# Kernel tuning notes

Measured on AMD Instinct MI355X. Metric: run time of the kernel, lower is better.

The kernel has to match this reference:

```python
import jax, jax.numpy as jnp
import numpy as np

N_NODES = 100000
N_EDGES = 1600000
IN_F, HID_F, OUT_F = 128, 128, 64


def setup_inputs() -> dict:
    key = jax.random.key(0)
    ks = jax.random.split(key, 10)
    x = jax.random.normal(ks[0], (N_NODES, IN_F), dtype=jnp.float32)
    adj_row = jax.random.randint(ks[1], (N_EDGES,), 0, N_NODES, dtype=jnp.int64)
    adj_col = jax.random.randint(ks[2], (N_EDGES,), 0, N_NODES, dtype=jnp.int64)
    adj_val = jax.random.uniform(ks[3], (N_EDGES,), dtype=jnp.float32)
    # layer weights (xavier-normal-ish scale), stored as [in, out]
    def w(k, fin, fout):
        return jax.random.normal(k, (fin, fout), dtype=jnp.float32) * jnp.sqrt(2.0 / (fin + fout))
    return {
        "x": x, "adj_row": adj_row, "adj_col": adj_col, "adj_val": adj_val,
        "W0": w(ks[4], IN_F, HID_F), "b0": jnp.zeros((HID_F,), jnp.float32),
        "W1": w(ks[5], HID_F, HID_F), "b1": jnp.zeros((HID_F,), jnp.float32),
        "W2": w(ks[6], HID_F, OUT_F), "b2": jnp.zeros((OUT_F,), jnp.float32),
    }


def _spmm(adj_row, adj_col, adj_val, h):
    # sparse [N,N] @ dense [N,F]: gather source rows, scale, scatter-add to dest
    msgs = adj_val[:, None] * h[adj_col]            # [E, F]
    return jax.ops.segment_sum(msgs, adj_row, num_segments=N_NODES)


def reference(x, adj_row, adj_col, adj_val, W0, b0, W1, b1, W2, b2):
    h = x
    params = [(W0, b0), (W1, b1), (W2, b2)]
    n_layers = len(params)
    for i, (W, b) in enumerate(params):
        h = h @ W + b                               # Linear
        h = _spmm(adj_row, adj_col, adj_val, h)     # torch.sparse.mm(adj, h)
        if i != n_layers - 1:
            h = jax.nn.relu(h)                      # activation on hidden layers only
    return h


if __name__ == "__main__":
    out = reference(**setup_inputs())
    print(out.shape)
```

## Files before the change

kernel.cpp:

```cpp
#include <hip/hip_runtime.h>
#include <hip/hip_bf16.h>

#define N_NODES 100000
#define N_EDGES 1600000

#define BIN_SHIFT 9
#define NBIN 196
#define NBLK 256
#define CHUNK 6250
#define SCAN_N (NBIN * NBLK)

typedef __attribute__((ext_vector_type(8))) short bf16x8;
typedef __attribute__((ext_vector_type(4))) float f32x4;

__device__ inline unsigned short f2bf(float f) {
    union { float f; unsigned u; } v; v.f = f;
    unsigned r = v.u + 0x7FFF + ((v.u >> 16) & 1);
    return (unsigned short)(r >> 16);
}
__device__ inline float bf2f(unsigned short h) {
    union { unsigned u; float f; } v; v.u = ((unsigned)h) << 16;
    return v.f;
}


__global__ __launch_bounds__(256) void p1_bincnt(const int* __restrict__ row,
                                                 int* __restrict__ cnt) {
    __shared__ int h[NBIN];
    for (int i = threadIdx.x; i < NBIN; i += 256) h[i] = 0;
    __syncthreads();
    int base = blockIdx.x * CHUNK;
    int end = base + CHUNK; if (end > N_EDGES) end = N_EDGES;
    for (int i = base + threadIdx.x; i < end; i += 256)
        atomicAdd(&h[row[i] >> BIN_SHIFT], 1);
    __syncthreads();
    for (int b = threadIdx.x; b < NBIN; b += 256)
        cnt[b * NBLK + blockIdx.x] = h[b];
}

__global__ __launch_bounds__(1024) void p2_scan(const int* __restrict__ cnt,
                                                int* __restrict__ base,
                                                int* __restrict__ rp) {
    __shared__ int s[1024];
    int t = threadIdx.x;
    const int per = SCAN_N / 1024;
    int lo = t * per, hi = lo + per;
    int sum = 0;
    for (int i = lo; i < hi; ++i) sum += cnt[i];
    s[t] = sum;
    __syncthreads();
    for (int off = 1; off < 1024; off <<= 1) {
        int v = (t >= off) ? s[t - off] : 0;
        __syncthreads();
        s[t] += v;
        __syncthreads();
    }
    int run = s[t] - sum;
    for (int i = lo; i < hi; ++i) { int c = cnt[i]; base[i] = run; run += c; }
    if (t == 0) rp[N_NODES] = N_EDGES;
}

__global__ __launch_bounds__(256) void p3_partition(const int* __restrict__ row,
                                                    const int* __restrict__ col,
                                                    const float* __restrict__ val,
                                                    const int* __restrict__ base,
                                                    int2* __restrict__ bout) {
    __shared__ int cur[NBIN];
    for (int i = threadIdx.x; i < NBIN; i += 256)
        cur[i] = base[i * NBLK + blockIdx.x];
    __syncthreads();
    int lo = blockIdx.x * CHUNK;
    int end = lo + CHUNK; if (end > N_EDGES) end = N_EDGES;
    for (int i = lo + threadIdx.x; i < end; i += 256) {
        int r = row[i];
        int b = r >> BIN_SHIFT;
        int p = atomicAdd(&cur[b], 1);
        int2 rec;
        rec.x = col[i] | ((r & 511) << 17);
        rec.y = __float_as_int(val[i]);
        bout[p] = rec;
    }
}

__global__ __launch_bounds__(256) void p4_binscatter(const int* __restrict__ base,
                                                     const int2* __restrict__ bin_in,
                                                     int* __restrict__ rp,
                                                     int2* __restrict__ erec) {
    __shared__ int cnt[512];
    __shared__ int part[256];
    const int b = blockIdx.x;
    const int t = threadIdx.x;
    const int lo = base[b * NBLK];
    const int hi = (b + 1 < NBIN) ? base[(b + 1) * NBLK] : N_EDGES;

    cnt[t] = 0; cnt[t + 256] = 0;
    __syncthreads();
    for (int e = lo + t; e < hi; e += 256)
        atomicAdd(&cnt[(unsigned)bin_in[e].x >> 17], 1);
    __syncthreads();

    int s0 = cnt[2 * t], s1 = cnt[2 * t + 1];
    int tsum = s0 + s1;
    part[t] = tsum;
    __syncthreads();
    for (int off = 1; off < 256; off <<= 1) {
        int v = (t >= off) ? part[t - off] : 0;
        __syncthreads();
        part[t] += v;
        __syncthreads();
    }
    int run = part[t] - tsum;
    cnt[2 * t] = run;
    cnt[2 * t + 1] = run + s0;

    const int rowbase = b << BIN_SHIFT;
    int r0 = rowbase + 2 * t, r1 = rowbase + 2 * t + 1;
    if (r0 < N_NODES) rp[r0] = lo + run;
    if (r1 < N_NODES) rp[r1] = lo + run + s0;
    __syncthreads();

    for (int e = lo + t; e < hi; e += 256) {
        int2 q = bin_in[e];
        int rl = (unsigned)q.x >> 17;
        int p = lo + atomicAdd(&cnt[rl], 1);
        int2 rec;
        rec.x = q.x & 0x1FFFF;
        rec.y = q.y;
        erec[p] = rec;
    }
}


template<int FOUT>
__global__ void pack_w_kernel(const float* __restrict__ W, unsigned short* __restrict__ Bp) {
    int idx = blockIdx.x * blockDim.x + threadIdx.x;
    if (idx >= FOUT * 128) return;
    int j = idx & 7, lane = (idx >> 3) & 63, kb = (idx >> 9) & 3, nt = idx >> 11;
    int k = kb * 32 + (lane >> 4) * 8 + j;
    int col = nt * 16 + (lane & 15);
    Bp[idx] = f2bf(W[k * FOUT + col]);
}


template<int FOUT, bool AF32>
__global__ __launch_bounds__(256) void gemm_mfma(const void* __restrict__ Xv,
                                                 const unsigned short* __restrict__ Bp,
                                                 const float* __restrict__ bias,
                                                 unsigned short* __restrict__ Y, int n) {
    const int wave = threadIdx.x >> 6;
    const int lane = threadIdx.x & 63;
    const int l15 = lane & 15, kg = lane >> 4;
    const int nbase = blockIdx.y * 64;
    const int rowTile = blockIdx.x * 128 + wave * 32;

    int r0 = rowTile + l15;      if (r0 >= n) r0 = n - 1;
    int r1 = rowTile + 16 + l15; if (r1 >= n) r1 = n - 1;

    bf16x8 a0[4], a1[4];
    if constexpr (AF32) {
        const float* x0 = (const float*)Xv + (size_t)r0 * 128 + kg * 8;
        const float* x1 = (const float*)Xv + (size_t)r1 * 128 + kg * 8;
        #pragma unroll
        for (int kb = 0; kb < 4; ++kb) {
            float4 u = *reinterpret_cast<const float4*>(x0 + kb * 32);
            float4 v = *reinterpret_cast<const float4*>(x0 + kb * 32 + 4);
            a0[kb] = (bf16x8){(short)f2bf(u.x), (short)f2bf(u.y), (short)f2bf(u.z), (short)f2bf(u.w),
                              (short)f2bf(v.x), (short)f2bf(v.y), (short)f2bf(v.z), (short)f2bf(v.w)};
            float4 p = *reinterpret_cast<const float4*>(x1 + kb * 32);
            float4 q = *reinterpret_cast<const float4*>(x1 + kb * 32 + 4);
            a1[kb] = (bf16x8){(short)f2bf(p.x), (short)f2bf(p.y), (short)f2bf(p.z), (short)f2bf(p.w),
                              (short)f2bf(q.x), (short)f2bf(q.y), (short)f2bf(q.z), (short)f2bf(q.w)};
        }
    } else {
        const bf16x8* x0 = reinterpret_cast<const bf16x8*>((const unsigned short*)Xv + (size_t)r0 * 128 + kg * 8);
        const bf16x8* x1 = reinterpret_cast<const bf16x8*>((const unsigned short*)Xv + (size_t)r1 * 128 + kg * 8);
        #pragma unroll
        for (int kb = 0; kb < 4; ++kb) { a0[kb] = x0[kb * 4]; a1[kb] = x1[kb * 4]; }
    }

    f32x4 c0[4], c1[4];
    #pragma unroll
    for (int t = 0; t < 4; ++t) {
        c0[t] = (f32x4){0.f, 0.f, 0.f, 0.f};
        c1[t] = (f32x4){0.f, 0.f, 0.f, 0.f};
    }

    const bf16x8* bpv = reinterpret_cast<const bf16x8*>(Bp);
    #pragma unroll
    for (int nt = 0; nt < 4; ++nt) {
        int ntAbs = (nbase >> 4) + nt;
        const bf16x8* bp = bpv + (size_t)(ntAbs * 4) * 64 + lane;
        #pragma unroll
        for (int kb = 0; kb < 4; ++kb) {
            bf16x8 b = bp[kb * 64];
            c0[nt] = __builtin_amdgcn_mfma_f32_16x16x32_bf16(a0[kb], b, c0[nt], 0, 0, 0);
            c1[nt] = __builtin_amdgcn_mfma_f32_16x16x32_bf16(a1[kb], b, c1[nt], 0, 0, 0);
        }
    }

    #pragma unroll
    for (int nt = 0; nt < 4; ++nt) {
        int col = nbase + nt * 16 + l15;
        float bv = bias[col];
        int rb = rowTile + kg * 4;
        #pragma unroll
        for (int j = 0; j < 4; ++j) {
            int ra = rb + j;
            if (ra < n) Y[(size_t)ra * FOUT + col] = f2bf(c0[nt][j] + bv);
            int rc = rb + 16 + j;
            if (rc < n) Y[(size_t)rc * FOUT + col] = f2bf(c1[nt][j] + bv);
        }
    }
}


__global__ __launch_bounds__(256) void spmm_mid(const int* __restrict__ rp,
                                                const int2* __restrict__ erec,
                                                const unsigned int* __restrict__ G,
                                                unsigned int* __restrict__ Y, int n) {
    int node = blockIdx.x * 4 + (threadIdx.x >> 6);
    if (node >= n) return;
    int f = threadIdx.x & 63;
    int e0 = rp[node], e1 = rp[node + 1];
    float acc0 = 0.f, acc1 = 0.f;
    const unsigned* Gf = G + f;
    int e = e0;
    for (; e + 4 <= e1; e += 4) {
        int2 q0 = erec[e], q1 = erec[e + 1], q2 = erec[e + 2], q3 = erec[e + 3];
        unsigned g0 = Gf[(size_t)q0.x * 64];
        unsigned g1 = Gf[(size_t)q1.x * 64];
        unsigned g2 = Gf[(size_t)q2.x * 64];
        unsigned g3 = Gf[(size_t)q3.x * 64];
        float v0 = __int_as_float(q0.y), v1 = __int_as_float(q1.y);
        float v2 = __int_as_float(q2.y), v3 = __int_as_float(q3.y);
        acc0 += v0 * bf2f((unsigned short)g0) + v1 * bf2f((unsigned short)g1)
              + v2 * bf2f((unsigned short)g2) + v3 * bf2f((unsigned short)g3);
        acc1 += v0 * bf2f((unsigned short)(g0 >> 16)) + v1 * bf2f((unsigned short)(g1 >> 16))
              + v2 * bf2f((unsigned short)(g2 >> 16)) + v3 * bf2f((unsigned short)(g3 >> 16));
    }
    for (; e < e1; ++e) {
        int2 q = erec[e];
        float v = __int_as_float(q.y);
        unsigned g = Gf[(size_t)q.x * 64];
        acc0 += v * bf2f((unsigned short)g);
        acc1 += v * bf2f((unsigned short)(g >> 16));
    }
    acc0 = fmaxf(acc0, 0.f); acc1 = fmaxf(acc1, 0.f);
    Y[(size_t)node * 64 + f] = (unsigned)f2bf(acc0) | ((unsigned)f2bf(acc1) << 16);
}

__global__ __launch_bounds__(256) void spmm_last(const int* __restrict__ rp,
                                                 const int2* __restrict__ erec,
                                                 const unsigned short* __restrict__ G,
                                                 float* __restrict__ Y, int n) {
    int node = blockIdx.x * 4 + (threadIdx.x >> 6);
    if (node >= n) return;
    int f = threadIdx.x & 63;
    int e0 = rp[node], e1 = rp[node + 1];
    float acc = 0.f;
    const unsigned short* Gf = G + f;
    int e = e0;
    for (; e + 4 <= e1; e += 4) {
        int2 q0 = erec[e], q1 = erec[e + 1], q2 = erec[e + 2], q3 = erec[e + 3];
        acc += __int_as_float(q0.y) * bf2f(Gf[(size_t)q0.x * 64])
             + __int_as_float(q1.y) * bf2f(Gf[(size_t)q1.x * 64])
             + __int_as_float(q2.y) * bf2f(Gf[(size_t)q2.x * 64])
             + __int_as_float(q3.y) * bf2f(Gf[(size_t)q3.x * 64]);
    }
    for (; e < e1; ++e) {
        int2 q = erec[e];
        acc += __int_as_float(q.y) * bf2f(Gf[(size_t)q.x * 64]);
    }
    Y[(size_t)node * 64 + f] = acc;
}


extern "C" void kernel_launch(void* const* d_in, const int* in_sizes, int n_in,
                              void* d_out, int out_size, void* d_ws, size_t ws_size,
                              hipStream_t stream) {
    const float* x    = (const float*)d_in[0];
    const int*   arow = (const int*)d_in[1];
    const int*   acol = (const int*)d_in[2];
    const float* aval = (const float*)d_in[3];
    const float* W0   = (const float*)d_in[4];
    const float* b0   = (const float*)d_in[5];
    const float* W1   = (const float*)d_in[6];
    const float* b1   = (const float*)d_in[7];
    const float* W2   = (const float*)d_in[8];
    const float* b2   = (const float*)d_in[9];
    float* out = (float*)d_out;

    unsigned short* hlin = (unsigned short*)d_ws;
    unsigned short* hact = hlin + (size_t)N_NODES * 128;
    unsigned short* Bp0  = hact + (size_t)N_NODES * 128;
    unsigned short* Bp1  = Bp0 + 128 * 128;
    unsigned short* Bp2  = Bp1 + 128 * 128;
    int* cnt   = (int*)(Bp2 + 64 * 128);
    int* base  = cnt + SCAN_N;
    int* rp    = base + SCAN_N;
    int2* bin_in = (int2*)(rp + N_NODES + 2);
    int2* erec   = bin_in + N_EDGES;

    p1_bincnt<<<NBLK, 256, 0, stream>>>(arow, cnt);
    p2_scan<<<1, 1024, 0, stream>>>(cnt, base, rp);
    p3_partition<<<NBLK, 256, 0, stream>>>(arow, acol, aval, base, bin_in);
    p4_binscatter<<<NBIN, 256, 0, stream>>>(base, bin_in, rp, erec);

    pack_w_kernel<128><<<64, 256, 0, stream>>>(W0, Bp0);
    pack_w_kernel<128><<<64, 256, 0, stream>>>(W1, Bp1);
    pack_w_kernel<64><<<32, 256, 0, stream>>>(W2, Bp2);

    dim3 gemm_grid((N_NODES + 127) / 128, 2);
    dim3 gemm_grid2((N_NODES + 127) / 128, 1);
    int spmm_grid = (N_NODES + 3) / 4;

    gemm_mfma<128, true><<<gemm_grid, 256, 0, stream>>>(x, Bp0, b0, hlin, N_NODES);
    spmm_mid<<<spmm_grid, 256, 0, stream>>>(rp, erec, (const unsigned*)hlin, (unsigned*)hact, N_NODES);
    gemm_mfma<128, false><<<gemm_grid, 256, 0, stream>>>(hact, Bp1, b1, hlin, N_NODES);
    spmm_mid<<<spmm_grid, 256, 0, stream>>>(rp, erec, (const unsigned*)hlin, (unsigned*)hact, N_NODES);
    gemm_mfma<64, false><<<gemm_grid2, 256, 0, stream>>>(hact, Bp2, b2, hlin, N_NODES);
    spmm_last<<<spmm_grid, 256, 0, stream>>>(rp, erec, hlin, out, N_NODES);
}
```

Before: 350.7 us.

## Fuse SpMM aggregation with following layer's MFMA GEMM through shared memory

Replaces the mid-layer spmm kernels and the following GEMMs with a fused kernel that aggregates 128 nodes' neighbor rows into an LDS tile (with ReLU and bf16 packing), then runs MFMA against the next weight matrix and writes the bf16 result directly. This removes one global write and read of the intermediate activation per layer and two kernel launches. The gather now uses wider 8-byte loads with edges split across two half-waves, combined by a lane shuffle, and spmm_last is restructured the same way. The trade-off is fewer blocks (one per 128 nodes) with serialized per-row gathers per wave and heavier LDS use per block, which may reduce latency hiding on the irregular gather.

```diff
diff --git a/kernel.cpp b/kernel.cpp
--- a/kernel.cpp
+++ b/kernel.cpp
@@ -130,7 +130,6 @@
     }
 }
 
-
 template<int FOUT>
 __global__ void pack_w_kernel(const float* __restrict__ W, unsigned short* __restrict__ Bp) {
     int idx = blockIdx.x * blockDim.x + threadIdx.x;
@@ -142,11 +141,11 @@
 }
 
 
-template<int FOUT, bool AF32>
-__global__ __launch_bounds__(256) void gemm_mfma(const void* __restrict__ Xv,
-                                                 const unsigned short* __restrict__ Bp,
-                                                 const float* __restrict__ bias,
-                                                 unsigned short* __restrict__ Y, int n) {
+template<int FOUT>
+__global__ __launch_bounds__(256) void gemm_mfma_f32A(const float* __restrict__ X,
+                                                      const unsigned short* __restrict__ Bp,
+                                                      const float* __restrict__ bias,
+                                                      unsigned short* __restrict__ Y, int n) {
     const int wave = threadIdx.x >> 6;
     const int lane = threadIdx.x & 63;
     const int l15 = lane & 15, kg = lane >> 4;
@@ -157,25 +156,18 @@
     int r1 = rowTile + 16 + l15; if (r1 >= n) r1 = n - 1;
 
     bf16x8 a0[4], a1[4];
-    if constexpr (AF32) {
-        const float* x0 = (const float*)Xv + (size_t)r0 * 128 + kg * 8;
-        const float* x1 = (const float*)Xv + (size_t)r1 * 128 + kg * 8;
-        #pragma unroll
-        for (int kb = 0; kb < 4; ++kb) {
-            float4 u = *reinterpret_cast<const float4*>(x0 + kb * 32);
-            float4 v = *reinterpret_cast<const float4*>(x0 + kb * 32 + 4);
-            a0[kb] = (bf16x8){(short)f2bf(u.x), (short)f2bf(u.y), (short)f2bf(u.z), (short)f2bf(u.w),
-                              (short)f2bf(v.x), (short)f2bf(v.y), (short)f2bf(v.z), (short)f2bf(v.w)};
-            float4 p = *reinterpret_cast<const float4*>(x1 + kb * 32);
-            float4 q = *reinterpret_cast<const float4*>(x1 + kb * 32 + 4);
-            a1[kb] = (bf16x8){(short)f2bf(p.x), (short)f2bf(p.y), (short)f2bf(p.z), (short)f2bf(p.w),
-                              (short)f2bf(q.x), (short)f2bf(q.y), (short)f2bf(q.z), (short)f2bf(q.w)};
-        }
-    } else {
-        const bf16x8* x0 = reinterpret_cast<const bf16x8*>((const unsigned short*)Xv + (size_t)r0 * 128 + kg * 8);
-        const bf16x8* x1 = reinterpret_cast<const bf16x8*>((const unsigned short*)Xv + (size_t)r1 * 128 + kg * 8);
-        #pragma unroll
-        for (int kb = 0; kb < 4; ++kb) { a0[kb] = x0[kb * 4]; a1[kb] = x1[kb * 4]; }
+    const float* x0 = X + (size_t)r0 * 128 + kg * 8;
+    const float* x1 = X + (size_t)r1 * 128 + kg * 8;
+    #pragma unroll
+    for (int kb = 0; kb < 4; ++kb) {
+        float4 u = *reinterpret_cast<const float4*>(x0 + kb * 32);
+        float4 v = *reinterpret_cast<const float4*>(x0 + kb * 32 + 4);
+        a0[kb] = (bf16x8){(short)f2bf(u.x), (short)f2bf(u.y), (short)f2bf(u.z), (short)f2bf(u.w),
+                          (short)f2bf(v.x), (short)f2bf(v.y), (short)f2bf(v.z), (short)f2bf(v.w)};
+        float4 p = *reinterpret_cast<const float4*>(x1 + kb * 32);
+        float4 q = *reinterpret_cast<const float4*>(x1 + kb * 32 + 4);
+        a1[kb] = (bf16x8){(short)f2bf(p.x), (short)f2bf(p.y), (short)f2bf(p.z), (short)f2bf(p.w),
+                          (short)f2bf(q.x), (short)f2bf(q.y), (short)f2bf(q.z), (short)f2bf(q.w)};
     }
 
     f32x4 c0[4], c1[4];
@@ -214,64 +206,132 @@
 }
 
 
-__global__ __launch_bounds__(256) void spmm_mid(const int* __restrict__ rp,
-                                                const int2* __restrict__ erec,
-                                                const unsigned int* __restrict__ G,
-                                                unsigned int* __restrict__ Y, int n) {
-    int node = blockIdx.x * 4 + (threadIdx.x >> 6);
-    if (node >= n) return;
-    int f = threadIdx.x & 63;
-    int e0 = rp[node], e1 = rp[node + 1];
-    float acc0 = 0.f, acc1 = 0.f;
-    const unsigned* Gf = G + f;
-    int e = e0;
-    for (; e + 4 <= e1; e += 4) {
-        int2 q0 = erec[e], q1 = erec[e + 1], q2 = erec[e + 2], q3 = erec[e + 3];
-        unsigned g0 = Gf[(size_t)q0.x * 64];
-        unsigned g1 = Gf[(size_t)q1.x * 64];
-        unsigned g2 = Gf[(size_t)q2.x * 64];
-        unsigned g3 = Gf[(size_t)q3.x * 64];
-        float v0 = __int_as_float(q0.y), v1 = __int_as_float(q1.y);
-        float v2 = __int_as_float(q2.y), v3 = __int_as_float(q3.y);
-        acc0 += v0 * bf2f((unsigned short)g0) + v1 * bf2f((unsigned short)g1)
-              + v2 * bf2f((unsigned short)g2) + v3 * bf2f((unsigned short)g3);
-        acc1 += v0 * bf2f((unsigned short)(g0 >> 16)) + v1 * bf2f((unsigned short)(g1 >> 16))
-              + v2 * bf2f((unsigned short)(g2 >> 16)) + v3 * bf2f((unsigned short)(g3 >> 16));
-    }
-    for (; e < e1; ++e) {
-        int2 q = erec[e];
-        float v = __int_as_float(q.y);
-        unsigned g = Gf[(size_t)q.x * 64];
-        acc0 += v * bf2f((unsigned short)g);
-        acc1 += v * bf2f((unsigned short)(g >> 16));
-    }
-    acc0 = fmaxf(acc0, 0.f); acc1 = fmaxf(acc1, 0.f);
-    Y[(size_t)node * 64 + f] = (unsigned)f2bf(acc0) | ((unsigned)f2bf(acc1) << 16);
-}
+template<int FOUT>
+__global__ __launch_bounds__(512, 4) void spmm_gemm_fused(const int* __restrict__ rp,
+                                                          const int2* __restrict__ erec,
+                                                          const unsigned* __restrict__ G,
+                                                          const unsigned short* __restrict__ Bp,
+                                                          const float* __restrict__ bias,
+                                                          unsigned short* __restrict__ Y,
+                                                          int n) {
+    __shared__ unsigned short A[128 * 136];
+    const int wave = threadIdx.x >> 6;
+    const int lane = threadIdx.x & 63;
+    const int half = lane >> 5;
+    const int f2 = lane & 31;
+    const int tile = blockIdx.x * 128;
+
+    for (int i = 0; i < 16; ++i) {
+        int lrow = wave * 16 + i;
+        int node = tile + lrow;
+        float a0 = 0.f, a1 = 0.f, a2 = 0.f, a3 = 0.f;
+        if (node < n) {
+            int e0 = rp[node], e1 = rp[node + 1];
+            int e = e0 + half;
+            for (; e + 3 <= e1; e += 4) {
+                int2 qa = erec[e], qb = erec[e + 2];
+                uint2 ga = *reinterpret_cast<const uint2*>(G + (size_t)qa.x * 64 + f2 * 2);
+                uint2 gb = *reinterpret_cast<const uint2*>(G + (size_t)qb.x * 64 + f2 * 2);
+                float va = __int_as_float(qa.y), vb = __int_as_float(qb.y);
+                a0 += va * bf2f((unsigned short)ga.x) + vb * bf2f((unsigned short)gb.x);
+                a1 += va * bf2f((unsigned short)(ga.x >> 16)) + vb * bf2f((unsigned short)(gb.x >> 16));
+                a2 += va * bf2f((unsigned short)ga.y) + vb * bf2f((unsigned short)gb.y);
+                a3 += va * bf2f((unsigned short)(ga.y >> 16)) + vb * bf2f((unsigned short)(gb.y >> 16));
+            }
+            if (e < e1) {
+                int2 q = erec[e];
+                uint2 g = *reinterpret_cast<const uint2*>(G + (size_t)q.x * 64 + f2 * 2);
+                float v = __int_as_float(q.y);
+                a0 += v * bf2f((unsigned short)g.x);
+                a1 += v * bf2f((unsigned short)(g.x >> 16));
+                a2 += v * bf2f((unsigned short)g.y);
+                a3 += v * bf2f((unsigned short)(g.y >> 16));
+            }
+        }
+        a0 += __shfl_xor(a0, 32);
+        a1 += __shfl_xor(a1, 32);
+        a2 += __shfl_xor(a2, 32);
+        a3 += __shfl_xor(a3, 32);
+        if (half == 0) {
+            a0 = fmaxf(a0, 0.f); a1 = fmaxf(a1, 0.f);
+            a2 = fmaxf(a2, 0.f); a3 = fmaxf(a3, 0.f);
+            unsigned p0 = (unsigned)f2bf(a0) | ((unsigned)f2bf(a1) << 16);
+            unsigned p1 = (unsigned)f2bf(a2) | ((unsigned)f2bf(a3) << 16);
+            uint2 pk; pk.x = p0; pk.y = p1;
+            *reinterpret_cast<uint2*>(&A[lrow * 136 + f2 * 4]) = pk;
+        }
+    }
+    __syncthreads();
+
+    const int l15 = lane & 15, kg = lane >> 4;
+    bf16x8 afr[4];
+    const unsigned short* arow = &A[(wave * 16 + l15) * 136 + kg * 8];
+    #pragma unroll
+    for (int kb = 0; kb < 4; ++kb)
+        afr[kb] = *reinterpret_cast<const bf16x8*>(arow + kb * 32);
+
+    constexpr int NT = FOUT / 16;
+    f32x4 c[NT];
+    #pragma unroll
+    for (int nt = 0; nt < NT; ++nt) c[nt] = (f32x4){0.f, 0.f, 0.f, 0.f};
+
+    const bf16x8* bpv = reinterpret_cast<const bf16x8*>(Bp);
+    #pragma unroll
+    for (int nt = 0; nt < NT; ++nt) {
+        const bf16x8* bp = bpv + (size_t)(nt * 4) * 64 + lane;
+        #pragma unroll
+        for (int kb = 0; kb < 4; ++kb)
+            c[nt] = __builtin_amdgcn_mfma_f32_16x16x32_bf16(afr[kb], bp[kb * 64], c[nt], 0, 0, 0);
+    }
+
+    #pragma unroll
+    for (int nt = 0; nt < NT; ++nt) {
+        int col = nt * 16 + l15;
+        float bv = bias[col];
+        int rb = tile + wave * 16 + kg * 4;
+        #pragma unroll
+        for (int j = 0; j < 4; ++j) {
+            int r = rb + j;
+            if (r < n) Y[(size_t)r * FOUT + col] = f2bf(c[nt][j] + bv);
+        }
+    }
+}
+
 
 __global__ __launch_bounds__(256) void spmm_last(const int* __restrict__ rp,
                                                  const int2* __restrict__ erec,
-                                                 const unsigned short* __restrict__ G,
+                                                 const unsigned* __restrict__ G,
                                                  float* __restrict__ Y, int n) {
     int node = blockIdx.x * 4 + (threadIdx.x >> 6);
     if (node >= n) return;
-    int f = threadIdx.x & 63;
+    int lane = threadIdx.x & 63;
+    int half = lane >> 5;
+    int f2 = lane & 31;
     int e0 = rp[node], e1 = rp[node + 1];
-    float acc = 0.f;
-    const unsigned short* Gf = G + f;
-    int e = e0;
-    for (; e + 4 <= e1; e += 4) {
-        int2 q0 = erec[e], q1 = erec[e + 1], q2 = erec[e + 2], q3 = erec[e + 3];
-        acc += __int_as_float(q0.y) * bf2f(Gf[(size_t)q0.x * 64])
-             + __int_as_float(q1.y) * bf2f(Gf[(size_t)q1.x * 64])
-             + __int_as_float(q2.y) * bf2f(Gf[(size_t)q2.x * 64])
-             + __int_as_float(q3.y) * bf2f(Gf[(size_t)q3.x * 64]);
-    }
-    for (; e < e1; ++e) {
+    float a0 = 0.f, a1 = 0.f;
+    const unsigned* Gf = G + f2;
+    int e = e0 + half;
+    for (; e + 3 <= e1; e += 4) {
+        int2 qa = erec[e], qb = erec[e + 2];
+        unsigned ga = Gf[(size_t)qa.x * 32];
+        unsigned gb = Gf[(size_t)qb.x * 32];
+        float va = __int_as_float(qa.y), vb = __int_as_float(qb.y);
+        a0 += va * bf2f((unsigned short)ga) + vb * bf2f((unsigned short)gb);
+        a1 += va * bf2f((unsigned short)(ga >> 16)) + vb * bf2f((unsigned short)(gb >> 16));
+    }
+    if (e < e1) {
         int2 q = erec[e];
-        acc += __int_as_float(q.y) * bf2f(Gf[(size_t)q.x * 64]);
-    }
-    Y[(size_t)node * 64 + f] = acc;
+        unsigned g = Gf[(size_t)q.x * 32];
+        float v = __int_as_float(q.y);
+        a0 += v * bf2f((unsigned short)g);
+        a1 += v * bf2f((unsigned short)(g >> 16));
+    }
+    a0 += __shfl_xor(a0, 32);
+    a1 += __shfl_xor(a1, 32);
+    if (half == 0) {
+        float2 o; o.x = a0; o.y = a1;
+        *reinterpret_cast<float2*>(&Y[(size_t)node * 64 + f2 * 2]) = o;
+    }
 }
 
 
@@ -290,9 +350,9 @@
     const float* b2   = (const float*)d_in[9];
     float* out = (float*)d_out;
 
-    unsigned short* hlin = (unsigned short*)d_ws;
-    unsigned short* hact = hlin + (size_t)N_NODES * 128;
-    unsigned short* Bp0  = hact + (size_t)N_NODES * 128;
+    unsigned short* hbuf0 = (unsigned short*)d_ws;
+    unsigned short* hbuf1 = hbuf0 + (size_t)N_NODES * 128;
+    unsigned short* Bp0  = hbuf1 + (size_t)N_NODES * 128;
     unsigned short* Bp1  = Bp0 + 128 * 128;
     unsigned short* Bp2  = Bp1 + 128 * 128;
     int* cnt   = (int*)(Bp2 + 64 * 128);
@@ -311,13 +371,11 @@
     pack_w_kernel<64><<<32, 256, 0, stream>>>(W2, Bp2);
 
     dim3 gemm_grid((N_NODES + 127) / 128, 2);
-    dim3 gemm_grid2((N_NODES + 127) / 128, 1);
+    int fused_grid = (N_NODES + 127) / 128;
     int spmm_grid = (N_NODES + 3) / 4;
 
-    gemm_mfma<128, true><<<gemm_grid, 256, 0, stream>>>(x, Bp0, b0, hlin, N_NODES);
-    spmm_mid<<<spmm_grid, 256, 0, stream>>>(rp, erec, (const unsigned*)hlin, (unsigned*)hact, N_NODES);
-    gemm_mfma<128, false><<<gemm_grid, 256, 0, stream>>>(hact, Bp1, b1, hlin, N_NODES);
-    spmm_mid<<<spmm_grid, 256, 0, stream>>>(rp, erec, (const unsigned*)hlin, (unsigned*)hact, N_NODES);
-    gemm_mfma<64, false><<<gemm_grid2, 256, 0, stream>>>(hact, Bp2, b2, hlin, N_NODES);
-    spmm_last<<<spmm_grid, 256, 0, stream>>>(rp, erec, hlin, out, N_NODES);
-}
+    gemm_mfma_f32A<128><<<gemm_grid, 256, 0, stream>>>(x, Bp0, b0, hbuf0, N_NODES);
+    spmm_gemm_fused<128><<<fused_grid, 512, 0, stream>>>(rp, erec, (const unsigned*)hbuf0, Bp1, b1, hbuf1, N_NODES);
+    spmm_gemm_fused<64><<<fused_grid, 512, 0, stream>>>(rp, erec, (const unsigned*)hbuf1, Bp2, b2, hbuf0, N_NODES);
+    spmm_last<<<spmm_grid, 256, 0, stream>>>(rp, erec, (const unsigned*)hbuf0, out, N_NODES);
+}
```

New measurement: 392.7 us. +12.0%, slower.

## Slice feature matrices into 16-column panels and compress edge records to 32 bits

Applied to the files above, without the earlier changes.

Intermediate activations are now stored in a sliced layout of 16-feature panels, each N×16 bf16, so the gather for a given panel reads a compact 32-byte row per source node and stays cache-resident. SpMM kernels process one panel per block, with 8 lanes per edge group and cross-lane shuffles to reduce partial sums. Edge records are packed into 32 bits (17-bit column plus 15-bit truncated bf16 value), which halves edge traffic but lowers the precision of the adjacency values. The three weight-packing launches are merged into one.

```diff
diff --git a/kernel.cpp b/kernel.cpp
--- a/kernel.cpp
+++ b/kernel.cpp
@@ -3,6 +3,8 @@
 
 #define N_NODES 100000
 #define N_EDGES 1600000
+#define N16 (N_NODES * 16)
+#define N8  (N_NODES * 8)
 
 #define BIN_SHIFT 9
 #define NBIN 196
@@ -20,6 +22,10 @@
 }
 __device__ inline float bf2f(unsigned short h) {
     union { unsigned u; float f; } v; v.u = ((unsigned)h) << 16;
+    return v.f;
+}
+__device__ inline float recval(unsigned q) {
+    union { unsigned u; float f; } v; v.u = (q & 0x7FFFu) << 17;
     return v.f;
 }
 
@@ -85,7 +91,7 @@
 __global__ __launch_bounds__(256) void p4_binscatter(const int* __restrict__ base,
                                                      const int2* __restrict__ bin_in,
                                                      int* __restrict__ rp,
-                                                     int2* __restrict__ erec) {
+                                                     unsigned* __restrict__ erec) {
     __shared__ int cnt[512];
     __shared__ int part[256];
     const int b = blockIdx.x;
@@ -123,26 +129,32 @@
         int2 q = bin_in[e];
         int rl = (unsigned)q.x >> 17;
         int p = lo + atomicAdd(&cnt[rl], 1);
-        int2 rec;
-        rec.x = q.x & 0x1FFFF;
-        rec.y = q.y;
+        unsigned rec = ((unsigned)(q.x & 0x1FFFF) << 15)
+                     | (((unsigned)f2bf(__int_as_float(q.y))) >> 1);
         erec[p] = rec;
     }
 }
 
 
-template<int FOUT>
-__global__ void pack_w_kernel(const float* __restrict__ W, unsigned short* __restrict__ Bp) {
-    int idx = blockIdx.x * blockDim.x + threadIdx.x;
-    if (idx >= FOUT * 128) return;
-    int j = idx & 7, lane = (idx >> 3) & 63, kb = (idx >> 9) & 3, nt = idx >> 11;
+__global__ __launch_bounds__(256) void pack_all(const float* __restrict__ W0,
+                                                const float* __restrict__ W1,
+                                                const float* __restrict__ W2,
+                                                unsigned short* __restrict__ Bp0,
+                                                unsigned short* __restrict__ Bp1,
+                                                unsigned short* __restrict__ Bp2) {
+    int idx = blockIdx.x * 256 + threadIdx.x;
+    const float* W; unsigned short* Bp; int fout, li;
+    if (idx < 16384)      { W = W0; Bp = Bp0; fout = 128; li = idx; }
+    else if (idx < 32768) { W = W1; Bp = Bp1; fout = 128; li = idx - 16384; }
+    else                  { W = W2; Bp = Bp2; fout = 64;  li = idx - 32768; }
+    int j = li & 7, lane = (li >> 3) & 63, kb = (li >> 9) & 3, nt = li >> 11;
     int k = kb * 32 + (lane >> 4) * 8 + j;
     int col = nt * 16 + (lane & 15);
-    Bp[idx] = f2bf(W[k * FOUT + col]);
-}
-
-
-template<int FOUT, bool AF32>
+    Bp[li] = f2bf(W[k * fout + col]);
+}
+
+
+template<int FOUT, int AMODE>
 __global__ __launch_bounds__(256) void gemm_mfma(const void* __restrict__ Xv,
                                                  const unsigned short* __restrict__ Bp,
                                                  const float* __restrict__ bias,
@@ -157,7 +169,7 @@
     int r1 = rowTile + 16 + l15; if (r1 >= n) r1 = n - 1;
 
     bf16x8 a0[4], a1[4];
-    if constexpr (AF32) {
+    if constexpr (AMODE == 0) {
         const float* x0 = (const float*)Xv + (size_t)r0 * 128 + kg * 8;
         const float* x1 = (const float*)Xv + (size_t)r1 * 128 + kg * 8;
         #pragma unroll
@@ -172,10 +184,13 @@
                               (short)f2bf(q.x), (short)f2bf(q.y), (short)f2bf(q.z), (short)f2bf(q.w)};
         }
     } else {
-        const bf16x8* x0 = reinterpret_cast<const bf16x8*>((const unsigned short*)Xv + (size_t)r0 * 128 + kg * 8);
-        const bf16x8* x1 = reinterpret_cast<const bf16x8*>((const unsigned short*)Xv + (size_t)r1 * 128 + kg * 8);
+        const unsigned short* Xs = (const unsigned short*)Xv;
         #pragma unroll
-        for (int kb = 0; kb < 4; ++kb) { a0[kb] = x0[kb * 4]; a1[kb] = x1[kb * 4]; }
+        for (int kb = 0; kb < 4; ++kb) {
+            const unsigned short* bse = Xs + (size_t)(kb * 2 + (kg >> 1)) * N16 + (kg & 1) * 8;
+            a0[kb] = *reinterpret_cast<const bf16x8*>(bse + (size_t)r0 * 16);
+            a1[kb] = *reinterpret_cast<const bf16x8*>(bse + (size_t)r1 * 16);
+        }
     }
 
     f32x4 c0[4], c1[4];
@@ -202,76 +217,110 @@
     for (int nt = 0; nt < 4; ++nt) {
         int col = nbase + nt * 16 + l15;
         float bv = bias[col];
+        unsigned short* yb = Y + (size_t)((nbase >> 4) + nt) * N16 + l15;
         int rb = rowTile + kg * 4;
         #pragma unroll
         for (int j = 0; j < 4; ++j) {
             int ra = rb + j;
-            if (ra < n) Y[(size_t)ra * FOUT + col] = f2bf(c0[nt][j] + bv);
+            if (ra < n) yb[(size_t)ra * 16] = f2bf(c0[nt][j] + bv);
             int rc = rb + 16 + j;
-            if (rc < n) Y[(size_t)rc * FOUT + col] = f2bf(c1[nt][j] + bv);
-        }
-    }
-}
-
-
-__global__ __launch_bounds__(256) void spmm_mid(const int* __restrict__ rp,
-                                                const int2* __restrict__ erec,
-                                                const unsigned int* __restrict__ G,
-                                                unsigned int* __restrict__ Y, int n) {
-    int node = blockIdx.x * 4 + (threadIdx.x >> 6);
-    if (node >= n) return;
-    int f = threadIdx.x & 63;
-    int e0 = rp[node], e1 = rp[node + 1];
-    float acc0 = 0.f, acc1 = 0.f;
-    const unsigned* Gf = G + f;
-    int e = e0;
-    for (; e + 4 <= e1; e += 4) {
-        int2 q0 = erec[e], q1 = erec[e + 1], q2 = erec[e + 2], q3 = erec[e + 3];
-        unsigned g0 = Gf[(size_t)q0.x * 64];
-        unsigned g1 = Gf[(size_t)q1.x * 64];
-        unsigned g2 = Gf[(size_t)q2.x * 64];
-        unsigned g3 = Gf[(size_t)q3.x * 64];
-        float v0 = __int_as_float(q0.y), v1 = __int_as_float(q1.y);
-        float v2 = __int_as_float(q2.y), v3 = __int_as_float(q3.y);
-        acc0 += v0 * bf2f((unsigned short)g0) + v1 * bf2f((unsigned short)g1)
-              + v2 * bf2f((unsigned short)g2) + v3 * bf2f((unsigned short)g3);
-        acc1 += v0 * bf2f((unsigned short)(g0 >> 16)) + v1 * bf2f((unsigned short)(g1 >> 16))
-              + v2 * bf2f((unsigned short)(g2 >> 16)) + v3 * bf2f((unsigned short)(g3 >> 16));
-    }
-    for (; e < e1; ++e) {
-        int2 q = erec[e];
-        float v = __int_as_float(q.y);
-        unsigned g = Gf[(size_t)q.x * 64];
-        acc0 += v * bf2f((unsigned short)g);
-        acc1 += v * bf2f((unsigned short)(g >> 16));
-    }
-    acc0 = fmaxf(acc0, 0.f); acc1 = fmaxf(acc1, 0.f);
-    Y[(size_t)node * 64 + f] = (unsigned)f2bf(acc0) | ((unsigned)f2bf(acc1) << 16);
-}
-
-__global__ __launch_bounds__(256) void spmm_last(const int* __restrict__ rp,
-                                                 const int2* __restrict__ erec,
-                                                 const unsigned short* __restrict__ G,
-                                                 float* __restrict__ Y, int n) {
-    int node = blockIdx.x * 4 + (threadIdx.x >> 6);
-    if (node >= n) return;
-    int f = threadIdx.x & 63;
-    int e0 = rp[node], e1 = rp[node + 1];
-    float acc = 0.f;
-    const unsigned short* Gf = G + f;
-    int e = e0;
-    for (; e + 4 <= e1; e += 4) {
-        int2 q0 = erec[e], q1 = erec[e + 1], q2 = erec[e + 2], q3 = erec[e + 3];
-        acc += __int_as_float(q0.y) * bf2f(Gf[(size_t)q0.x * 64])
-             + __int_as_float(q1.y) * bf2f(Gf[(size_t)q1.x * 64])
-             + __int_as_float(q2.y) * bf2f(Gf[(size_t)q2.x * 64])
-             + __int_as_float(q3.y) * bf2f(Gf[(size_t)q3.x * 64]);
-    }
-    for (; e < e1; ++e) {
-        int2 q = erec[e];
-        acc += __int_as_float(q.y) * bf2f(Gf[(size_t)q.x * 64]);
-    }
-    Y[(size_t)node * 64 + f] = acc;
+            if (rc < n) yb[(size_t)rc * 16] = f2bf(c1[nt][j] + bv);
+        }
+    }
+}
+
+
+__global__ __launch_bounds__(256) void spmm_mid_sliced(const int* __restrict__ rp,
+                                                       const unsigned* __restrict__ erec,
+                                                       const unsigned* __restrict__ G,
+                                                       unsigned* __restrict__ Y,
+                                                       int n) {
+    const int slice = blockIdx.x & 7;
+    const int grp = blockIdx.x >> 3;
+    const int wave = threadIdx.x >> 6;
+    const int lane = threadIdx.x & 63;
+    const int sub = lane & 7;
+    const int eg = lane >> 3;
+    const unsigned* Gs = G + (size_t)slice * N8 + sub;
+    unsigned* Ys = Y + (size_t)slice * N8 + sub;
+    const int node0 = grp * 32 + wave * 8;
+
+    for (int i = 0; i < 8; ++i) {
+        int node = node0 + i;
+        if (node >= n) return;
+        int e0 = rp[node], e1 = rp[node + 1];
+        float f0 = 0.f, f1 = 0.f;
+        int e = e0 + eg;
+        for (; e + 8 < e1; e += 16) {
+            unsigned qa = __builtin_nontemporal_load(erec + e);
+            unsigned qb = __builtin_nontemporal_load(erec + e + 8);
+            unsigned ga = Gs[(size_t)(qa >> 15) * 8];
+            unsigned gb = Gs[(size_t)(qb >> 15) * 8];
+            float va = recval(qa), vb = recval(qb);
+            f0 += va * bf2f((unsigned short)ga) + vb * bf2f((unsigned short)gb);
+            f1 += va * bf2f((unsigned short)(ga >> 16)) + vb * bf2f((unsigned short)(gb >> 16));
+        }
+        if (e < e1) {
+            unsigned q = __builtin_nontemporal_load(erec + e);
+            unsigned g = Gs[(size_t)(q >> 15) * 8];
+            float v = recval(q);
+            f0 += v * bf2f((unsigned short)g);
+            f1 += v * bf2f((unsigned short)(g >> 16));
+        }
+        f0 += __shfl_xor(f0, 8);  f0 += __shfl_xor(f0, 16);  f0 += __shfl_xor(f0, 32);
+        f1 += __shfl_xor(f1, 8);  f1 += __shfl_xor(f1, 16);  f1 += __shfl_xor(f1, 32);
+        if (eg == 0) {
+            f0 = fmaxf(f0, 0.f); f1 = fmaxf(f1, 0.f);
+            unsigned pk = (unsigned)f2bf(f0) | ((unsigned)f2bf(f1) << 16);
+            __builtin_nontemporal_store(pk, Ys + (size_t)node * 8);
+        }
+    }
+}
+
+
+__global__ __launch_bounds__(256) void spmm_last_sliced(const int* __restrict__ rp,
+                                                        const unsigned* __restrict__ erec,
+                                                        const unsigned* __restrict__ G,
+                                                        float* __restrict__ out,
+                                                        int n) {
+    const int slice = blockIdx.x & 3;
+    const int grp = blockIdx.x >> 2;
+    const int wave = threadIdx.x >> 6;
+    const int lane = threadIdx.x & 63;
+    const int sub = lane & 7;
+    const int eg = lane >> 3;
+    const unsigned* Gs = G + (size_t)slice * N8 + sub;
+    const int node0 = grp * 32 + wave * 8;
+
+    for (int i = 0; i < 8; ++i) {
+        int node = node0 + i;
+        if (node >= n) return;
+        int e0 = rp[node], e1 = rp[node + 1];
+        float f0 = 0.f, f1 = 0.f;
+        int e = e0 + eg;
+        for (; e + 8 < e1; e += 16) {
+            unsigned qa = __builtin_nontemporal_load(erec + e);
+            unsigned qb = __builtin_nontemporal_load(erec + e + 8);
+            unsigned ga = Gs[(size_t)(qa >> 15) * 8];
+            unsigned gb = Gs[(size_t)(qb >> 15) * 8];
+            float va = recval(qa), vb = recval(qb);
+            f0 += va * bf2f((unsigned short)ga) + vb * bf2f((unsigned short)gb);
+            f1 += va * bf2f((unsigned short)(ga >> 16)) + vb * bf2f((unsigned short)(gb >> 16));
+        }
+        if (e < e1) {
+            unsigned q = __builtin_nontemporal_load(erec + e);
+            unsigned g = Gs[(size_t)(q >> 15) * 8];
+            float v = recval(q);
+            f0 += v * bf2f((unsigned short)g);
+            f1 += v * bf2f((unsigned short)(g >> 16));
+        }
+        f0 += __shfl_xor(f0, 8);  f0 += __shfl_xor(f0, 16);  f0 += __shfl_xor(f0, 32);
+        f1 += __shfl_xor(f1, 8);  f1 += __shfl_xor(f1, 16);  f1 += __shfl_xor(f1, 32);
+        if (eg == 0) {
+            float2 o; o.x = f0; o.y = f1;
+            *reinterpret_cast<float2*>(&out[(size_t)node * 64 + slice * 16 + sub * 2]) = o;
+        }
+    }
 }
 
 
@@ -290,34 +339,34 @@
     const float* b2   = (const float*)d_in[9];
     float* out = (float*)d_out;
 
-    unsigned short* hlin = (unsigned short*)d_ws;
-    unsigned short* hact = hlin + (size_t)N_NODES * 128;
-    unsigned short* Bp0  = hact + (size_t)N_NODES * 128;
-    unsigned short* Bp1  = Bp0 + 128 * 128;
-    unsigned short* Bp2  = Bp1 + 128 * 128;
-    int* cnt   = (int*)(Bp2 + 64 * 128);
-    int* base  = cnt + SCAN_N;
-    int* rp    = base + SCAN_N;
-    int2* bin_in = (int2*)(rp + N_NODES + 2);
-    int2* erec   = bin_in + N_EDGES;
+    unsigned short* S0  = (unsigned short*)d_ws;
+    unsigned short* S1  = S0 + (size_t)N_NODES * 128;
+    unsigned short* S2  = S1 + (size_t)N_NODES * 128;
+    unsigned short* Bp0 = S2 + (size_t)N_NODES * 64;
+    unsigned short* Bp1 = Bp0 + 16384;
+    unsigned short* Bp2 = Bp1 + 16384;
+    int* cnt  = (int*)(Bp2 + 8192);
+    int* base = cnt + SCAN_N;
+    int* rp   = base + SCAN_N;
+    int2* bin_in  = (int2*)(rp + N_NODES + 2);
+    unsigned* erec = (unsigned*)(bin_in + N_EDGES);
 
     p1_bincnt<<<NBLK, 256, 0, stream>>>(arow, cnt);
     p2_scan<<<1, 1024, 0, stream>>>(cnt, base, rp);
     p3_partition<<<NBLK, 256, 0, stream>>>(arow, acol, aval, base, bin_in);
     p4_binscatter<<<NBIN, 256, 0, stream>>>(base, bin_in, rp, erec);
 
-    pack_w_kernel<128><<<64, 256, 0, stream>>>(W0, Bp0);
-    pack_w_kernel<128><<<64, 256, 0, stream>>>(W1, Bp1);
-    pack_w_kernel<64><<<32, 256, 0, stream>>>(W2, Bp2);
+    pack_all<<<160, 256, 0, stream>>>(W0, W1, W2, Bp0, Bp1, Bp2);
 
     dim3 gemm_grid((N_NODES + 127) / 128, 2);
     dim3 gemm_grid2((N_NODES + 127) / 128, 1);
-    int spmm_grid = (N_NODES + 3) / 4;
-
-    gemm_mfma<128, true><<<gemm_grid, 256, 0, stream>>>(x, Bp0, b0, hlin, N_NODES);
-    spmm_mid<<<spmm_grid, 256, 0, stream>>>(rp, erec, (const unsigned*)hlin, (unsigned*)hact, N_NODES);
-    gemm_mfma<128, false><<<gemm_grid, 256, 0, stream>>>(hact, Bp1, b1, hlin, N_NODES);
-    spmm_mid<<<spmm_grid, 256, 0, stream>>>(rp, erec, (const unsigned*)hlin, (unsigned*)hact, N_NODES);
-    gemm_mfma<64, false><<<gemm_grid2, 256, 0, stream>>>(hact, Bp2, b2, hlin, N_NODES);
-    spmm_last<<<spmm_grid, 256, 0, stream>>>(rp, erec, hlin, out, N_NODES);
-}
+    int spmm_grid = 8 * ((N_NODES + 31) / 32);
+    int last_grid = 4 * ((N_NODES + 31) / 32);
+
+    gemm_mfma<128, 0><<<gemm_grid, 256, 0, stream>>>(x, Bp0, b0, S0, N_NODES);
+    spmm_mid_sliced<<<spmm_grid, 256, 0, stream>>>(rp, erec, (const unsigned*)S0, (unsigned*)S1, N_NODES);
+    gemm_mfma<128, 1><<<gemm_grid, 256, 0, stream>>>(S1, Bp1, b1, S0, N_NODES);
+    spmm_mid_sliced<<<spmm_grid, 256, 0, stream>>>(rp, erec, (const unsigned*)S0, (unsigned*)S1, N_NODES);
+    gemm_mfma<64, 1><<<gemm_grid2, 256, 0, stream>>>(S1, Bp2, b2, S2, N_NODES);
+    spmm_last_sliced<<<last_grid, 256, 0, stream>>>(rp, erec, (const unsigned*)S2, out, N_NODES);
+}
```

Measured after the change: 705.5 us. 101% more time.

## Cooperatively load edge records and broadcast via readlane in SpMM kernels

Applied to the files above, without the earlier changes.

The SpMM kernels now load up to 64 edge records per wave with one coalesced load and broadcast each column index and value through readlane, instead of every lane re-reading the same records. The last-layer SpMM packs two bf16 features per lane and splits the wave into two halves that process alternate edges, then combines them with a cross-half shuffle and a float2 store. The three weight-packing launches are also merged into one. This trades redundant record loads and narrow 16-bit gathers for extra readlane scalar work and some control flow.

```diff
diff --git a/kernel.cpp b/kernel.cpp
--- a/kernel.cpp
+++ b/kernel.cpp
@@ -131,14 +131,21 @@
 }
 
 
-template<int FOUT>
-__global__ void pack_w_kernel(const float* __restrict__ W, unsigned short* __restrict__ Bp) {
-    int idx = blockIdx.x * blockDim.x + threadIdx.x;
-    if (idx >= FOUT * 128) return;
-    int j = idx & 7, lane = (idx >> 3) & 63, kb = (idx >> 9) & 3, nt = idx >> 11;
+__global__ __launch_bounds__(256) void pack_all(const float* __restrict__ W0,
+                                                const float* __restrict__ W1,
+                                                const float* __restrict__ W2,
+                                                unsigned short* __restrict__ Bp0,
+                                                unsigned short* __restrict__ Bp1,
+                                                unsigned short* __restrict__ Bp2) {
+    int idx = blockIdx.x * 256 + threadIdx.x;
+    const float* W; unsigned short* Bp; int fout, li;
+    if (idx < 16384)      { W = W0; Bp = Bp0; fout = 128; li = idx; }
+    else if (idx < 32768) { W = W1; Bp = Bp1; fout = 128; li = idx - 16384; }
+    else                  { W = W2; Bp = Bp2; fout = 64;  li = idx - 32768; }
+    int j = li & 7, lane = (li >> 3) & 63, kb = (li >> 9) & 3, nt = li >> 11;
     int k = kb * 32 + (lane >> 4) * 8 + j;
     int col = nt * 16 + (lane & 15);
-    Bp[idx] = f2bf(W[k * FOUT + col]);
+    Bp[li] = f2bf(W[k * fout + col]);
 }
 
 
@@ -216,62 +223,107 @@
 
 __global__ __launch_bounds__(256) void spmm_mid(const int* __restrict__ rp,
                                                 const int2* __restrict__ erec,
-                                                const unsigned int* __restrict__ G,
-                                                unsigned int* __restrict__ Y, int n) {
+                                                const unsigned* __restrict__ G,
+                                                unsigned* __restrict__ Y, int n) {
     int node = blockIdx.x * 4 + (threadIdx.x >> 6);
     if (node >= n) return;
-    int f = threadIdx.x & 63;
+    int lane = threadIdx.x & 63;
     int e0 = rp[node], e1 = rp[node + 1];
-    float acc0 = 0.f, acc1 = 0.f;
-    const unsigned* Gf = G + f;
-    int e = e0;
-    for (; e + 4 <= e1; e += 4) {
-        int2 q0 = erec[e], q1 = erec[e + 1], q2 = erec[e + 2], q3 = erec[e + 3];
-        unsigned g0 = Gf[(size_t)q0.x * 64];
-        unsigned g1 = Gf[(size_t)q1.x * 64];
-        unsigned g2 = Gf[(size_t)q2.x * 64];
-        unsigned g3 = Gf[(size_t)q3.x * 64];
-        float v0 = __int_as_float(q0.y), v1 = __int_as_float(q1.y);
-        float v2 = __int_as_float(q2.y), v3 = __int_as_float(q3.y);
-        acc0 += v0 * bf2f((unsigned short)g0) + v1 * bf2f((unsigned short)g1)
-              + v2 * bf2f((unsigned short)g2) + v3 * bf2f((unsigned short)g3);
-        acc1 += v0 * bf2f((unsigned short)(g0 >> 16)) + v1 * bf2f((unsigned short)(g1 >> 16))
-              + v2 * bf2f((unsigned short)(g2 >> 16)) + v3 * bf2f((unsigned short)(g3 >> 16));
-    }
-    for (; e < e1; ++e) {
-        int2 q = erec[e];
-        float v = __int_as_float(q.y);
-        unsigned g = Gf[(size_t)q.x * 64];
-        acc0 += v * bf2f((unsigned short)g);
-        acc1 += v * bf2f((unsigned short)(g >> 16));
-    }
-    acc0 = fmaxf(acc0, 0.f); acc1 = fmaxf(acc1, 0.f);
-    Y[(size_t)node * 64 + f] = (unsigned)f2bf(acc0) | ((unsigned)f2bf(acc1) << 16);
-}
+    float a0 = 0.f, a1 = 0.f;
+    const unsigned* Gf = G + lane;
+    while (e0 < e1) {
+        int take = e1 - e0; if (take > 64) take = 64;
+        int2 rec = erec[e0 + (lane < take ? lane : take - 1)];
+        int i = 0;
+        for (; i + 8 <= take; i += 8) {
+            unsigned g[8]; float v[8];
+            #pragma unroll
+            for (int j = 0; j < 8; ++j) {
+                int c = __builtin_amdgcn_readlane(rec.x, i + j);
+                v[j] = __int_as_float(__builtin_amdgcn_readlane(rec.y, i + j));
+                g[j] = Gf[(size_t)c * 64];
+            }
+            #pragma unroll
+            for (int j = 0; j < 8; ++j) {
+                a0 += v[j] * bf2f((unsigned short)g[j]);
+                a1 += v[j] * bf2f((unsigned short)(g[j] >> 16));
+            }
+        }
+        for (; i < take; ++i) {
+            int c = __builtin_amdgcn_readlane(rec.x, i);
+            float v = __int_as_float(__builtin_amdgcn_readlane(rec.y, i));
+            unsigned g = Gf[(size_t)c * 64];
+            a0 += v * bf2f((unsigned short)g);
+            a1 += v * bf2f((unsigned short)(g >> 16));
+        }
+        e0 += take;
+    }
+    a0 = fmaxf(a0, 0.f); a1 = fmaxf(a1, 0.f);
+    Y[(size_t)node * 64 + lane] = (unsigned)f2bf(a0) | ((unsigned)f2bf(a1) << 16);
+}
+
 
 __global__ __launch_bounds__(256) void spmm_last(const int* __restrict__ rp,
                                                  const int2* __restrict__ erec,
-                                                 const unsigned short* __restrict__ G,
-                                                 float* __restrict__ Y, int n) {
+                                                 const unsigned* __restrict__ G,
+                                                 float* __restrict__ out, int n) {
     int node = blockIdx.x * 4 + (threadIdx.x >> 6);
     if (node >= n) return;
-    int f = threadIdx.x & 63;
+    int lane = threadIdx.x & 63;
+    int s = lane & 31, h = lane >> 5;
     int e0 = rp[node], e1 = rp[node + 1];
-    float acc = 0.f;
-    const unsigned short* Gf = G + f;
-    int e = e0;
-    for (; e + 4 <= e1; e += 4) {
-        int2 q0 = erec[e], q1 = erec[e + 1], q2 = erec[e + 2], q3 = erec[e + 3];
-        acc += __int_as_float(q0.y) * bf2f(Gf[(size_t)q0.x * 64])
-             + __int_as_float(q1.y) * bf2f(Gf[(size_t)q1.x * 64])
-             + __int_as_float(q2.y) * bf2f(Gf[(size_t)q2.x * 64])
-             + __int_as_float(q3.y) * bf2f(Gf[(size_t)q3.x * 64]);
-    }
-    for (; e < e1; ++e) {
-        int2 q = erec[e];
-        acc += __int_as_float(q.y) * bf2f(Gf[(size_t)q.x * 64]);
-    }
-    Y[(size_t)node * 64 + f] = acc;
+    float a0 = 0.f, a1 = 0.f;
+    const unsigned* Gf = G + s;
+    while (e0 < e1) {
+        int take = e1 - e0; if (take > 64) take = 64;
+        int2 rec = erec[e0 + (lane < take ? lane : take - 1)];
+        int i = 0;
+        for (; i + 16 <= take; i += 16) {
+            unsigned g[8]; float v[8];
+            #pragma unroll
+            for (int j = 0; j < 8; ++j) {
+                int idx = i + 2 * j;
+                int ca = __builtin_amdgcn_readlane(rec.x, idx);
+                int cb = __builtin_amdgcn_readlane(rec.x, idx + 1);
+                float va = __int_as_float(__builtin_amdgcn_readlane(rec.y, idx));
+                float vb = __int_as_float(__builtin_amdgcn_readlane(rec.y, idx + 1));
+                int c = h ? cb : ca;
+                v[j] = h ? vb : va;
+                g[j] = Gf[(size_t)c * 32];
+            }
+            #pragma unroll
+            for (int j = 0; j < 8; ++j) {
+                a0 += v[j] * bf2f((unsigned short)g[j]);
+                a1 += v[j] * bf2f((unsigned short)(g[j] >> 16));
+            }
+        }
+        for (; i + 2 <= take; i += 2) {
+            int ca = __builtin_amdgcn_readlane(rec.x, i);
+            int cb = __builtin_amdgcn_readlane(rec.x, i + 1);
+            float va = __int_as_float(__builtin_amdgcn_readlane(rec.y, i));
+            float vb = __int_as_float(__builtin_amdgcn_readlane(rec.y, i + 1));
+            int c = h ? cb : ca;
+            float v = h ? vb : va;
+            unsigned g = Gf[(size_t)c * 32];
+            a0 += v * bf2f((unsigned short)g);
+            a1 += v * bf2f((unsigned short)(g >> 16));
+        }
+        if (i < take) {
+            int c = __builtin_amdgcn_readlane(rec.x, i);
+            float v = __int_as_float(__builtin_amdgcn_readlane(rec.y, i));
+            v = h ? 0.f : v;
+            unsigned g = Gf[(size_t)c * 32];
+            a0 += v * bf2f((unsigned short)g);
+            a1 += v * bf2f((unsigned short)(g >> 16));
+        }
+        e0 += take;
+    }
+    a0 += __shfl_xor(a0, 32);
+    a1 += __shfl_xor(a1, 32);
+    if (h == 0) {
+        float2 o; o.x = a0; o.y = a1;
+        *reinterpret_cast<float2*>(&out[(size_t)node * 64 + s * 2]) = o;
+    }
 }
 
 
@@ -293,11 +345,11 @@
     unsigned short* hlin = (unsigned short*)d_ws;
     unsigned short* hact = hlin + (size_t)N_NODES * 128;
     unsigned short* Bp0  = hact + (size_t)N_NODES * 128;
-    unsigned short* Bp1  = Bp0 + 128 * 128;
-    unsigned short* Bp2  = Bp1 + 128 * 128;
-    int* cnt   = (int*)(Bp2 + 64 * 128);
-    int* base  = cnt + SCAN_N;
-    int* rp    = base + SCAN_N;
+    unsigned short* Bp1  = Bp0 + 16384;
+    unsigned short* Bp2  = Bp1 + 16384;
+    int* cnt  = (int*)(Bp2 + 8192);
+    int* base = cnt + SCAN_N;
+    int* rp   = base + SCAN_N;
     int2* bin_in = (int2*)(rp + N_NODES + 2);
     int2* erec   = bin_in + N_EDGES;
 
@@ -306,9 +358,7 @@
     p3_partition<<<NBLK, 256, 0, stream>>>(arow, acol, aval, base, bin_in);
     p4_binscatter<<<NBIN, 256, 0, stream>>>(base, bin_in, rp, erec);
 
-    pack_w_kernel<128><<<64, 256, 0, stream>>>(W0, Bp0);
-    pack_w_kernel<128><<<64, 256, 0, stream>>>(W1, Bp1);
-    pack_w_kernel<64><<<32, 256, 0, stream>>>(W2, Bp2);
+    pack_all<<<160, 256, 0, stream>>>(W0, W1, W2, Bp0, Bp1, Bp2);
 
     dim3 gemm_grid((N_NODES + 127) / 128, 2);
     dim3 gemm_grid2((N_NODES + 127) / 128, 1);
@@ -319,5 +369,5 @@
     gemm_mfma<128, false><<<gemm_grid, 256, 0, stream>>>(hact, Bp1, b1, hlin, N_NODES);
     spmm_mid<<<spmm_grid, 256, 0, stream>>>(rp, erec, (const unsigned*)hlin, (unsigned*)hact, N_NODES);
     gemm_mfma<64, false><<<gemm_grid2, 256, 0, stream>>>(hact, Bp2, b2, hlin, N_NODES);
-    spmm_last<<<spmm_grid, 256, 0, stream>>>(rp, erec, hlin, out, N_NODES);
-}
+    spmm_last<<<spmm_grid, 256, 0, stream>>>(rp, erec, (const unsigned*)hlin, out, N_NODES);
+}
```

Measured after the change: 312.9 us. 1.12x faster.
